# Kernel optimization log

Measured on AMD Instinct MI355X. Metric: run time of the kernel, lower is better.

## Reference

```python
import jax, jax.numpy as jnp
import numpy as np

NUM_STEPS = 2  # consensus iterations


def psi3(r, edge_index, W3, b3):
    # one-layer message passing GNN: sum-aggregate neighbors, add self, linear, relu
    src, dst = edge_index[0], edge_index[1]
    agg = jnp.zeros_like(r).at[dst].add(r[src])
    return jax.nn.relu((r + agg) @ W3 + b3)


def setup_inputs() -> dict:
    key = jax.random.key(0)
    ks = jax.random.split(key, 12)
    N_total, C_in = 4096, 128   # global entity table
    N_s, N_t = 1024, 1024       # source / target graph sizes (B=1)
    E = 16384                   # edges per graph (avg degree 16)
    C1, C2 = 256, 256           # psi_1 / psi_2 output dims
    R = 32                      # psi_3 in_channels == out_channels
    s_in = 1.0 / np.sqrt(C_in)
    s_r = 1.0 / np.sqrt(R)
    inp = {}
    inp['inputs'] = jax.random.normal(ks[0], (N_total, C_in), jnp.float32)
    inp['index_n1'] = jax.random.randint(ks[1], (N_s,), 0, N_total)
    inp['index_n2'] = jax.random.randint(ks[2], (N_t,), 0, N_total)
    inp['edge_index_s'] = jax.random.randint(ks[3], (2, E), 0, N_s)
    inp['edge_index_t'] = jax.random.randint(ks[4], (2, E), 0, N_t)
    # psi_1 / psi_2: linear entity encoders
    inp['W1'] = jax.random.uniform(ks[5], (C_in, C1), jnp.float32, -s_in, s_in)
    inp['W2'] = jax.random.uniform(ks[6], (C_in, C2), jnp.float32, -s_in, s_in)
    # psi_3 weights
    inp['W3'] = jax.random.uniform(ks[7], (R, R), jnp.float32, -s_r, s_r)
    inp['b3'] = jnp.zeros((R,), jnp.float32)
    # consensus MLP: R -> R -> 1
    inp['Wm1'] = jax.random.uniform(ks[8], (R, R), jnp.float32, -s_r, s_r)
    inp['bm1'] = jnp.zeros((R,), jnp.float32)
    inp['Wm2'] = jax.random.uniform(ks[9], (R, 1), jnp.float32, -s_r, s_r)
    inp['bm2'] = jnp.zeros((1,), jnp.float32)
    # random node indicator functions r_s for each consensus step (drawn
    # with torch.randn inside the original forward; precomputed here)
    inp['rs_all'] = jax.random.normal(ks[10], (NUM_STEPS, N_s, R), jnp.float32)
    return inp


def reference(inputs, index_n1, index_n2, edge_index_s, edge_index_t,
              W1, W2, W3, b3, Wm1, bm1, Wm2, bm2, rs_all):
    time_emb = inputs @ W1  # psi_1
    rel_emb = inputs @ W2   # psi_2
    # h = cat(time, rel) per node; B=1 so masks are all-true
    h_s = jnp.concatenate([time_emb[index_n1], rel_emb[index_n1]], axis=-1)  # [N_s, C1+C2]
    h_t = jnp.concatenate([time_emb[index_n2], rel_emb[index_n2]], axis=-1)  # [N_t, C1+C2]
    S_hat = h_s @ h_t.T  # [N_s, N_t] dense similarity
    S_0 = jax.nn.softmax(S_hat, axis=-1)  # masked_softmax with full mask

    def step(S_hat, r_s):
        S = jax.nn.softmax(S_hat, axis=-1)
        r_t = S.T @ r_s                                  # [N_t, R]
        o_s = psi3(r_s, edge_index_s, W3, b3)            # [N_s, R]
        o_t = psi3(r_t, edge_index_t, W3, b3)            # [N_t, R]
        D = o_s[:, None, :] - o_t[None, :, :]            # [N_s, N_t, R]
        delta = (jax.nn.relu(D @ Wm1 + bm1) @ Wm2 + bm2)[..., 0]  # mlp(D).squeeze(-1)
        return S_hat + delta, None

    S_hat, _ = jax.lax.scan(step, S_hat, rs_all)
    S_L = jax.nn.softmax(S_hat, axis=-1)
    return S_0, S_L
```

## Files before the change

kernel.cpp:

```cpp
#include <hip/hip_runtime.h>
#include <math.h>

#define N_S   1024
#define N_T   1024
#define E_EDG 16384
#define R     32
#define NSTEP 2

__global__ __launch_bounds__(256) void k_pre(const float* __restrict__ W1,
                                             const float* __restrict__ W2,
                                             float* __restrict__ G,
                                             float* __restrict__ zbuf) {
    const int t = threadIdx.x, bid = blockIdx.x;
    if (bid >= 128) {
        ((float4*)zbuf)[(bid - 128) * 256 + t] = make_float4(0.f, 0.f, 0.f, 0.f);
        return;
    }
    __shared__ float wa[512];
    __shared__ float wt[64][129];
    __shared__ float red[256];
    const int a = bid;
    for (int s = t; s < 512; s += 256)
        wa[s] = (s < 256) ? W1[a * 256 + s] : W2[a * 256 + (s - 256)];
    __syncthreads();
    float acc = 0.f;
    const int b = t & 127, h = t >> 7;
    for (int ci = 0; ci < 8; ++ci) {
        const float* Wsrc = (ci < 4) ? W1 : W2;
        const int cbase = (ci & 3) * 64;
#pragma unroll
        for (int it = 0; it < 8; ++it) {
            int s = it * 256 + t;
            int br = s >> 4, q = s & 15;
            float4 v = *(const float4*)(Wsrc + (size_t)br * 256 + cbase + q * 4);
            wt[q * 4 + 0][br] = v.x; wt[q * 4 + 1][br] = v.y;
            wt[q * 4 + 2][br] = v.z; wt[q * 4 + 3][br] = v.w;
        }
        __syncthreads();
        const float* wac = wa + ci * 64 + h * 32;
#pragma unroll
        for (int cc = 0; cc < 32; ++cc)
            acc += wac[cc] * wt[h * 32 + cc][b];
        __syncthreads();
    }
    red[t] = acc;
    __syncthreads();
    if (t < 128) G[a * 128 + t] = red[t] + red[t + 128];
}

__global__ __launch_bounds__(256) void k_build(
    const float* __restrict__ X, const int* __restrict__ idx1,
    const int* __restrict__ idx2, const int* __restrict__ es,
    const float* __restrict__ rs_all, const float* __restrict__ G,
    float* aggs0, float* aggs1,
    float* __restrict__ Shat, float2* __restrict__ part) {
    __shared__ float As[64][132];
    union U { float Xs[64][128]; float Bs[64][132]; };
    __shared__ U u;
    const int t = threadIdx.x, bid = blockIdx.x;
    const int i0 = (bid >> 4) * 64, j0 = (bid & 15) * 64, jt = bid & 15;

    for (int v = bid * 256 + t; v < 2 * E_EDG * 32; v += 65536) {
        int k = v & 31, ei = v >> 5;
        int step = ei >> 14, e = ei & (E_EDG - 1);
        int src = es[e], dst = es[E_EDG + e];
        const float* rs = rs_all + (size_t)step * N_S * R;
        float* aggs = step ? aggs1 : aggs0;
        atomicAdd(&aggs[(size_t)dst * 32 + k], rs[(size_t)src * 32 + k]);
    }

    for (int s = t; s < 64 * 32; s += 256) {
        int row = s >> 5, q = s & 31;
        *(float4*)&u.Xs[row][q * 4] =
            ((const float4*)(X + (size_t)idx1[i0 + row] * 128))[q];
    }
    __syncthreads();

    {
        const int a = t & 127, h = t >> 7;
        float acc[32];
#pragma unroll
        for (int r = 0; r < 32; ++r) acc[r] = 0.f;
        for (int dq = 0; dq < 32; ++dq) {
            const float* gp = G + dq * 4 * 128 + a;
            float g0 = gp[0], g1 = gp[128], g2 = gp[256], g3 = gp[384];
#pragma unroll
            for (int r = 0; r < 32; ++r) {
                float4 x = *(const float4*)&u.Xs[h * 32 + r][dq * 4];
                acc[r] += x.x * g0 + x.y * g1 + x.z * g2 + x.w * g3;
            }
        }
#pragma unroll
        for (int r = 0; r < 32; ++r) As[h * 32 + r][a] = acc[r];
    }
    __syncthreads();

    for (int s = t; s < 64 * 32; s += 256) {
        int row = s >> 5, q = s & 31;
        *(float4*)&u.Bs[row][q * 4] =
            ((const float4*)(X + (size_t)idx2[j0 + row] * 128))[q];
    }
    __syncthreads();

    const int r = t >> 4, c = t & 15;
    float acc[4][4] = {};
    for (int k = 0; k < 128; k += 4) {
        float4 ya[4], xb[4];
#pragma unroll
        for (int a2 = 0; a2 < 4; ++a2) ya[a2] = *(const float4*)&As[r + 16 * a2][k];
#pragma unroll
        for (int b2 = 0; b2 < 4; ++b2) xb[b2] = *(const float4*)&u.Bs[c + 16 * b2][k];
#pragma unroll
        for (int a2 = 0; a2 < 4; ++a2)
#pragma unroll
            for (int b2 = 0; b2 < 4; ++b2)
                acc[a2][b2] += ya[a2].x * xb[b2].x + ya[a2].y * xb[b2].y +
                               ya[a2].z * xb[b2].z + ya[a2].w * xb[b2].w;
    }
#pragma unroll
    for (int a2 = 0; a2 < 4; ++a2) {
#pragma unroll
        for (int b2 = 0; b2 < 4; ++b2)
            Shat[(size_t)(i0 + r + 16 * a2) * 1024 + (j0 + c + 16 * b2)] = acc[a2][b2];
        float M = fmaxf(fmaxf(acc[a2][0], acc[a2][1]), fmaxf(acc[a2][2], acc[a2][3]));
#pragma unroll
        for (int m = 1; m < 16; m <<= 1) M = fmaxf(M, __shfl_xor(M, m, 16));
        float Ss = 0.f;
#pragma unroll
        for (int b2 = 0; b2 < 4; ++b2) Ss += __expf(acc[a2][b2] - M);
#pragma unroll
        for (int m = 1; m < 16; m <<= 1) Ss += __shfl_xor(Ss, m, 16);
        if (c == 0)
            part[(size_t)(i0 + r + 16 * a2) * 16 + jt] = make_float2(M, Ss);
    }
}

__global__ __launch_bounds__(256) void k_rt(const float* __restrict__ Shat,
                                            const float2* __restrict__ part,
                                            const float* __restrict__ rs,
                                            float* __restrict__ rt,
                                            float* __restrict__ out0) {
    int j0 = blockIdx.x * 64;
    int i0 = blockIdx.y * 128;
    int t = threadIdx.x;
    __shared__ float Sl[16][68];
    __shared__ float Rl[16][36];
    __shared__ float mrow[128], irow[128];
    if (t < 128) {
        const float2* pr = part + (size_t)(i0 + t) * 16;
        float M = -1e30f, S = 0.f;
        float2 ps[16];
#pragma unroll
        for (int q = 0; q < 16; ++q) { ps[q] = pr[q]; M = fmaxf(M, ps[q].x); }
#pragma unroll
        for (int q = 0; q < 16; ++q) S += ps[q].y * __expf(ps[q].x - M);
        mrow[t] = M;
        irow[t] = 1.f / S;
    }
    __syncthreads();
    int k = t & 31, jg = t >> 5;
    float acc[8] = {};
    for (int ic = 0; ic < 128; ic += 16) {
        for (int s = t; s < 16 * 16; s += 256) {
            int row = s >> 4, q = s & 15;
            int lr = ic + row;
            float4 v = ((const float4*)(Shat + (size_t)(i0 + lr) * 1024 + j0))[q];
            float m = mrow[lr], inv = irow[lr];
            v.x = __expf(v.x - m) * inv;
            v.y = __expf(v.y - m) * inv;
            v.z = __expf(v.z - m) * inv;
            v.w = __expf(v.w - m) * inv;
            *(float4*)&Sl[row][q * 4] = v;
            if (out0)
                ((float4*)(out0 + (size_t)(i0 + lr) * 1024 + j0))[q] = v;
        }
        for (int s = t; s < 16 * 8; s += 256) {
            int row = s >> 3, q = s & 7;
            *(float4*)&Rl[row][q * 4] =
                ((const float4*)(rs + (size_t)(i0 + ic + row) * 32))[q];
        }
        __syncthreads();
#pragma unroll
        for (int ii = 0; ii < 16; ++ii) {
            float rv = Rl[ii][k];
#pragma unroll
            for (int m = 0; m < 8; ++m)
                acc[m] += Sl[ii][jg * 8 + m] * rv;
        }
        __syncthreads();
    }
#pragma unroll
    for (int m = 0; m < 8; ++m)
        atomicAdd(&rt[(size_t)(j0 + jg * 8 + m) * 32 + k], acc[m]);
}

__global__ __launch_bounds__(256) void k_scat_t(const int* __restrict__ et,
                                                const float* __restrict__ rt,
                                                float* __restrict__ aggt) {
    int gid = blockIdx.x * 256 + threadIdx.x;
    int k = gid & 31;
    int e = gid >> 5;
    int src = et[e], dst = et[E_EDG + e];
    atomicAdd(&aggt[(size_t)dst * 32 + k], rt[(size_t)src * 32 + k]);
}

__global__ __launch_bounds__(256) void k_delta(
    const float* __restrict__ rs, const float* __restrict__ aggs,
    const float* __restrict__ rt, const float* __restrict__ aggt,
    const float* __restrict__ W3, const float* __restrict__ b3,
    const float* __restrict__ Wm1, const float* __restrict__ bm1,
    const float* __restrict__ Wm2, const float* __restrict__ bm2,
    float* __restrict__ Shat, float2* __restrict__ part) {
    __shared__ float us[64][33], uq[64][33];
    __shared__ float olP[64][33], olQ[64][33];
    __shared__ float Pl[64][36], Ql[64][36];
    const int t = threadIdx.x;
    const int bx = blockIdx.x, by = blockIdx.y;
    const int i0 = by * 64, j0 = bx * 64;
    const int k = t & 31, team = t >> 5;

    float w3r[32], wm1r[32];
#pragma unroll
    for (int m = 0; m < 32; ++m) {
        w3r[m]  = W3[m * 32 + k];
        wm1r[m] = Wm1[m * 32 + k];
    }
    const float b3k = b3[k], bm1k = bm1[k], bv = bm2[0];

    for (int s = t; s < 64 * 8; s += 256) {
        int row = s >> 3, q = s & 7;
        float4 a4 = ((const float4*)(rs + (size_t)(i0 + row) * 32))[q];
        float4 b4 = ((const float4*)(aggs + (size_t)(i0 + row) * 32))[q];
        a4.x += b4.x; a4.y += b4.y; a4.z += b4.z; a4.w += b4.w;
        *(float4*)&us[row][q * 4] = a4;
        float4 c4 = ((const float4*)(rt + (size_t)(j0 + row) * 32))[q];
        float4 d4 = ((const float4*)(aggt + (size_t)(j0 + row) * 32))[q];
        c4.x += d4.x; c4.y += d4.y; c4.z += d4.z; c4.w += d4.w;
        *(float4*)&uq[row][q * 4] = c4;
    }
    __syncthreads();

#pragma unroll
    for (int p = 0; p < 8; ++p) {
        const int row = p * 8 + team;
        float a1 = b3k, a2 = b3k;
#pragma unroll
        for (int m = 0; m < 32; ++m) {
            a1 += us[row][m] * w3r[m];
            a2 += uq[row][m] * w3r[m];
        }
        olP[row][k] = fmaxf(a1, 0.f);
        olQ[row][k] = fmaxf(a2, 0.f);
    }
    __syncthreads();

#pragma unroll
    for (int p = 0; p < 8; ++p) {
        const int row = p * 8 + team;
        float a1 = bm1k, a2 = 0.f;
#pragma unroll
        for (int m = 0; m < 32; ++m) {
            a1 += olP[row][m] * wm1r[m];
            a2 += olQ[row][m] * wm1r[m];
        }
        Pl[row][k] = a1;
        Ql[row][k] = a2;
    }
    __syncthreads();

    const int r = t >> 4, c = t & 15;
    float acc[4][4] = {};
#pragma unroll
    for (int q = 0; q < 8; ++q) {
        float4 w = ((const float4*)Wm2)[q];
        float4 pa[4], qb[4];
#pragma unroll
        for (int a = 0; a < 4; ++a) pa[a] = *(const float4*)&Pl[r + 16 * a][q * 4];
#pragma unroll
        for (int b = 0; b < 4; ++b) qb[b] = *(const float4*)&Ql[c + 16 * b][q * 4];
#pragma unroll
        for (int a = 0; a < 4; ++a)
#pragma unroll
            for (int b = 0; b < 4; ++b)
                acc[a][b] += w.x * fmaxf(pa[a].x - qb[b].x, 0.f)
                           + w.y * fmaxf(pa[a].y - qb[b].y, 0.f)
                           + w.z * fmaxf(pa[a].z - qb[b].z, 0.f)
                           + w.w * fmaxf(pa[a].w - qb[b].w, 0.f);
    }
#pragma unroll
    for (int a = 0; a < 4; ++a) {
        float v[4];
#pragma unroll
        for (int b = 0; b < 4; ++b) {
            size_t idx = (size_t)(i0 + r + 16 * a) * 1024 + (j0 + c + 16 * b);
            v[b] = Shat[idx] + acc[a][b] + bv;
            Shat[idx] = v[b];
        }
        float M = fmaxf(fmaxf(v[0], v[1]), fmaxf(v[2], v[3]));
#pragma unroll
        for (int m = 1; m < 16; m <<= 1) M = fmaxf(M, __shfl_xor(M, m, 16));
        float Ss = 0.f;
#pragma unroll
        for (int b = 0; b < 4; ++b) Ss += __expf(v[b] - M);
#pragma unroll
        for (int m = 1; m < 16; m <<= 1) Ss += __shfl_xor(Ss, m, 16);
        if (c == 0)
            part[(size_t)(i0 + r + 16 * a) * 16 + bx] = make_float2(M, Ss);
    }
}

__global__ __launch_bounds__(256) void k_fsm(const float* __restrict__ Shat,
                                             const float2* __restrict__ part,
                                             float* __restrict__ out2) {
    int i = blockIdx.x, t = threadIdx.x;
    const float2* pr = part + (size_t)i * 16;
    float M = -1e30f, S = 0.f;
    float2 ps[16];
#pragma unroll
    for (int q = 0; q < 16; ++q) { ps[q] = pr[q]; M = fmaxf(M, ps[q].x); }
#pragma unroll
    for (int q = 0; q < 16; ++q) S += ps[q].y * __expf(ps[q].x - M);
    float inv = 1.f / S;
    const float* row = Shat + (size_t)i * 1024;
#pragma unroll
    for (int j = 0; j < 4; ++j)
        out2[(size_t)i * 1024 + t + 256 * j] = __expf(row[t + 256 * j] - M) * inv;
}

extern "C" void kernel_launch(void* const* d_in, const int* in_sizes, int n_in,
                              void* d_out, int out_size, void* d_ws, size_t ws_size,
                              hipStream_t stream) {
    const float* inputs = (const float*)d_in[0];
    const int*   idx1   = (const int*)d_in[1];
    const int*   idx2   = (const int*)d_in[2];
    const int*   es     = (const int*)d_in[3];
    const int*   et     = (const int*)d_in[4];
    const float* W1     = (const float*)d_in[5];
    const float* W2     = (const float*)d_in[6];
    const float* W3     = (const float*)d_in[7];
    const float* b3     = (const float*)d_in[8];
    const float* Wm1    = (const float*)d_in[9];
    const float* bm1    = (const float*)d_in[10];
    const float* Wm2    = (const float*)d_in[11];
    const float* bm2    = (const float*)d_in[12];
    const float* rs_all = (const float*)d_in[13];
    float* out = (float*)d_out;
    float* ws  = (float*)d_ws;

    float*  Shat  = ws;
    float*  G     = Shat + (1 << 20);
    float2* part  = (float2*)(G + 16384);
    float*  rt0   = G + 16384 + 32768;
    float*  rt1   = rt0 + 32768;
    float*  aggs0 = rt1 + 32768;
    float*  aggs1 = aggs0 + 32768;
    float*  aggt0 = aggs1 + 32768;
    float*  aggt1 = aggt0 + 32768;

    k_pre<<<320, 256, 0, stream>>>(W1, W2, G, rt0);
    k_build<<<256, 256, 0, stream>>>(inputs, idx1, idx2, es, rs_all, G,
                                     aggs0, aggs1, Shat, part);
    for (int step = 0; step < NSTEP; ++step) {
        const float* rs   = rs_all + (size_t)step * N_S * R;
        float*       rtS  = step ? rt1 : rt0;
        float*       aggtS= step ? aggt1 : aggt0;
        const float* aggsS= step ? aggs1 : aggs0;
        k_rt<<<dim3(16, 8), 256, 0, stream>>>(Shat, part, rs, rtS,
                                              step == 0 ? out : nullptr);
        k_scat_t<<<2048, 256, 0, stream>>>(et, rtS, aggtS);
        k_delta<<<dim3(16, 16), 256, 0, stream>>>(rs, aggsS, rtS, aggtS,
                                                  W3, b3, Wm1, bm1, Wm2, bm2,
                                                  Shat, part);
    }
    k_fsm<<<1024, 256, 0, stream>>>(Shat, part, out + (1 << 20));
}
```

Baseline: 211.9 us.

## Split build kernel to compute source projection once instead of per tile

The fused build kernel recomputed the projection of each source row through G in all 16 column tiles. It is now split into k_ys, which computes Ys = X[idx1]·G once per source row and also performs the edge scatter, and k_shat, which runs the similarity GEMM plus partial softmax statistics from Ys. This removes the 16x redundant projection work but adds an extra kernel launch and a global round trip for Ys.

```diff
diff --git a/kernel.cpp b/kernel.cpp
--- a/kernel.cpp
+++ b/kernel.cpp
@@ -48,19 +48,27 @@
     if (t < 128) G[a * 128 + t] = red[t] + red[t + 128];
 }
 
-__global__ __launch_bounds__(256) void k_build(
-    const float* __restrict__ X, const int* __restrict__ idx1,
-    const int* __restrict__ idx2, const int* __restrict__ es,
-    const float* __restrict__ rs_all, const float* __restrict__ G,
-    float* aggs0, float* aggs1,
-    float* __restrict__ Shat, float2* __restrict__ part) {
-    __shared__ float As[64][132];
-    union U { float Xs[64][128]; float Bs[64][132]; };
-    __shared__ U u;
-    const int t = threadIdx.x, bid = blockIdx.x;
-    const int i0 = (bid >> 4) * 64, j0 = (bid & 15) * 64, jt = bid & 15;
-
-    for (int v = bid * 256 + t; v < 2 * E_EDG * 32; v += 65536) {
+__global__ __launch_bounds__(128) void k_ys(const float* __restrict__ X,
+                                            const int* __restrict__ idx1,
+                                            const float* __restrict__ G,
+                                            const int* __restrict__ es,
+                                            const float* __restrict__ rs_all,
+                                            float* aggs0, float* aggs1,
+                                            float* __restrict__ Ys) {
+    int i = blockIdx.x;
+    int a = threadIdx.x;
+    __shared__ float x[128];
+    int row = idx1[i];
+    x[a] = X[(size_t)row * 128 + a];
+    __syncthreads();
+    float acc = 0.f;
+#pragma unroll 8
+    for (int d = 0; d < 128; ++d)
+        acc += x[d] * G[d * 128 + a];
+    Ys[(size_t)i * 128 + a] = acc;
+
+    int gid = i * 128 + a;
+    for (int v = gid; v < 2 * E_EDG * 32; v += 131072) {
         int k = v & 31, ei = v >> 5;
         int step = ei >> 14, e = ei & (E_EDG - 1);
         int src = es[e], dst = es[E_EDG + e];
@@ -68,70 +76,59 @@
         float* aggs = step ? aggs1 : aggs0;
         atomicAdd(&aggs[(size_t)dst * 32 + k], rs[(size_t)src * 32 + k]);
     }
-
+}
+
+__global__ __launch_bounds__(256) void k_shat(const float* __restrict__ Ys,
+                                              const float* __restrict__ X,
+                                              const int* __restrict__ idx2,
+                                              float* __restrict__ Shat,
+                                              float2* __restrict__ part) {
+    __shared__ float As[64][132];
+    __shared__ float Bs[64][132];
+    const int i0 = blockIdx.y * 64, j0 = blockIdx.x * 64, jt = blockIdx.x;
+    const int t = threadIdx.x;
     for (int s = t; s < 64 * 32; s += 256) {
         int row = s >> 5, q = s & 31;
-        *(float4*)&u.Xs[row][q * 4] =
-            ((const float4*)(X + (size_t)idx1[i0 + row] * 128))[q];
-    }
-    __syncthreads();
-
-    {
-        const int a = t & 127, h = t >> 7;
-        float acc[32];
-#pragma unroll
-        for (int r = 0; r < 32; ++r) acc[r] = 0.f;
-        for (int dq = 0; dq < 32; ++dq) {
-            const float* gp = G + dq * 4 * 128 + a;
-            float g0 = gp[0], g1 = gp[128], g2 = gp[256], g3 = gp[384];
-#pragma unroll
-            for (int r = 0; r < 32; ++r) {
-                float4 x = *(const float4*)&u.Xs[h * 32 + r][dq * 4];
-                acc[r] += x.x * g0 + x.y * g1 + x.z * g2 + x.w * g3;
-            }
-        }
-#pragma unroll
-        for (int r = 0; r < 32; ++r) As[h * 32 + r][a] = acc[r];
-    }
-    __syncthreads();
-
+        *(float4*)&As[row][q * 4] =
+            ((const float4*)(Ys + (size_t)(i0 + row) * 128))[q];
+    }
     for (int s = t; s < 64 * 32; s += 256) {
         int row = s >> 5, q = s & 31;
-        *(float4*)&u.Bs[row][q * 4] =
-            ((const float4*)(X + (size_t)idx2[j0 + row] * 128))[q];
-    }
-    __syncthreads();
-
+        int src = idx2[j0 + row];
+        *(float4*)&Bs[row][q * 4] =
+            ((const float4*)(X + (size_t)src * 128))[q];
+    }
+    __syncthreads();
     const int r = t >> 4, c = t & 15;
     float acc[4][4] = {};
     for (int k = 0; k < 128; k += 4) {
         float4 ya[4], xb[4];
 #pragma unroll
-        for (int a2 = 0; a2 < 4; ++a2) ya[a2] = *(const float4*)&As[r + 16 * a2][k];
-#pragma unroll
-        for (int b2 = 0; b2 < 4; ++b2) xb[b2] = *(const float4*)&u.Bs[c + 16 * b2][k];
-#pragma unroll
-        for (int a2 = 0; a2 < 4; ++a2)
-#pragma unroll
-            for (int b2 = 0; b2 < 4; ++b2)
-                acc[a2][b2] += ya[a2].x * xb[b2].x + ya[a2].y * xb[b2].y +
-                               ya[a2].z * xb[b2].z + ya[a2].w * xb[b2].w;
-    }
-#pragma unroll
-    for (int a2 = 0; a2 < 4; ++a2) {
-#pragma unroll
-        for (int b2 = 0; b2 < 4; ++b2)
-            Shat[(size_t)(i0 + r + 16 * a2) * 1024 + (j0 + c + 16 * b2)] = acc[a2][b2];
-        float M = fmaxf(fmaxf(acc[a2][0], acc[a2][1]), fmaxf(acc[a2][2], acc[a2][3]));
+        for (int a = 0; a < 4; ++a) ya[a] = *(const float4*)&As[r + 16 * a][k];
+#pragma unroll
+        for (int b = 0; b < 4; ++b) xb[b] = *(const float4*)&Bs[c + 16 * b][k];
+#pragma unroll
+        for (int a = 0; a < 4; ++a)
+#pragma unroll
+            for (int b = 0; b < 4; ++b)
+                acc[a][b] += ya[a].x * xb[b].x + ya[a].y * xb[b].y +
+                             ya[a].z * xb[b].z + ya[a].w * xb[b].w;
+    }
+#pragma unroll
+    for (int a = 0; a < 4; ++a) {
+#pragma unroll
+        for (int b = 0; b < 4; ++b)
+            Shat[(size_t)(i0 + r + 16 * a) * 1024 + (j0 + c + 16 * b)] = acc[a][b];
+        float M = fmaxf(fmaxf(acc[a][0], acc[a][1]), fmaxf(acc[a][2], acc[a][3]));
 #pragma unroll
         for (int m = 1; m < 16; m <<= 1) M = fmaxf(M, __shfl_xor(M, m, 16));
         float Ss = 0.f;
 #pragma unroll
-        for (int b2 = 0; b2 < 4; ++b2) Ss += __expf(acc[a2][b2] - M);
+        for (int b = 0; b < 4; ++b) Ss += __expf(acc[a][b] - M);
 #pragma unroll
         for (int m = 1; m < 16; m <<= 1) Ss += __shfl_xor(Ss, m, 16);
         if (c == 0)
-            part[(size_t)(i0 + r + 16 * a2) * 16 + jt] = make_float2(M, Ss);
+            part[(size_t)(i0 + r + 16 * a) * 16 + jt] = make_float2(M, Ss);
     }
 }
 
@@ -348,7 +345,8 @@
     float* ws  = (float*)d_ws;
 
     float*  Shat  = ws;
-    float*  G     = Shat + (1 << 20);
+    float*  Ys    = Shat + (1 << 20);
+    float*  G     = Ys + 131072;
     float2* part  = (float2*)(G + 16384);
     float*  rt0   = G + 16384 + 32768;
     float*  rt1   = rt0 + 32768;
@@ -358,13 +356,14 @@
     float*  aggt1 = aggt0 + 32768;
 
     k_pre<<<320, 256, 0, stream>>>(W1, W2, G, rt0);
-    k_build<<<256, 256, 0, stream>>>(inputs, idx1, idx2, es, rs_all, G,
-                                     aggs0, aggs1, Shat, part);
+    k_ys<<<1024, 128, 0, stream>>>(inputs, idx1, G, es, rs_all,
+                                   aggs0, aggs1, Ys);
+    k_shat<<<dim3(16, 16), 256, 0, stream>>>(Ys, inputs, idx2, Shat, part);
     for (int step = 0; step < NSTEP; ++step) {
-        const float* rs   = rs_all + (size_t)step * N_S * R;
-        float*       rtS  = step ? rt1 : rt0;
-        float*       aggtS= step ? aggt1 : aggt0;
-        const float* aggsS= step ? aggs1 : aggs0;
+        const float* rs    = rs_all + (size_t)step * N_S * R;
+        float*       rtS   = step ? rt1 : rt0;
+        float*       aggtS = step ? aggt1 : aggt0;
+        const float* aggsS = step ? aggs1 : aggs0;
         k_rt<<<dim3(16, 8), 256, 0, stream>>>(Shat, part, rs, rtS,
                                               step == 0 ? out : nullptr);
         k_scat_t<<<2048, 256, 0, stream>>>(et, rtS, aggtS);
```

Result: faster. 187.9 us (-11.4%).
